# Optimization experiments

Measured on AMD Instinct MI355X. Metric: run time of the kernel, lower is better.

The kernel has to match this reference:

```python
import jax, jax.numpy as jnp
import numpy as np

B, N, C, K = 8, 4096, 128, 16
POOL_RATE = 4  # npoint = N // POOL_RATE


def setup_inputs() -> dict:
    key = jax.random.key(0)
    k1, k2, k3 = jax.random.split(key, 3)
    vertices = jax.random.normal(k1, (B, 3, N), dtype=jnp.float32)
    feature_map = jax.random.normal(k2, (B, C, N), dtype=jnp.float32)
    # pre-flattened global knn indices, values in [0, B*N) as produced upstream
    idx = jax.random.randint(k3, (B * N * K,), 0, B * N, dtype=jnp.int64)
    return {"vertices": vertices, "feature_map": feature_map, "idx": idx}


def farthest_point_sample(xyz, npoint):
    """xyz: (B, N, 3) -> centroid indices (B, npoint).
    Deterministic start at index 0 (torch version uses a random start)."""
    b, n, _ = xyz.shape

    def step(carry, _):
        distance, farthest = carry
        centroid = jnp.take_along_axis(xyz, farthest[:, None, None], axis=1)  # (B,1,3)
        dist = jnp.sum((xyz - centroid) ** 2, axis=-1)  # (B,N)
        distance = jnp.minimum(distance, dist)
        new_farthest = jnp.argmax(distance, axis=-1)
        return (distance, new_farthest), farthest

    dist0 = jnp.full((b, n), 1e10, dtype=xyz.dtype)
    far0 = jnp.zeros((b,), dtype=jnp.int32)
    _, cents = jax.lax.scan(step, (dist0, far0), None, length=npoint)
    return cents.T  # (B, npoint)


def reference(vertices, feature_map, idx):
    b, c, n = feature_map.shape
    # get_graph_feature with precomputed flat idx: gather neighbors then max-pool
    flat = feature_map.transpose(0, 2, 1).reshape(b * n, c)        # (B*N, C)
    neigh = flat[idx].reshape(b, n, K, c)                          # (B,N,K,C)
    pooled = jnp.max(neigh, axis=2)                                # (B,N,C) == (B,C,N) pooled_feature, channel-last

    npoint = n // POOL_RATE
    xyz = vertices.transpose(0, 2, 1)                              # (B,N,3)
    cents = farthest_point_sample(xyz, npoint)                     # (B,npoint)

    vertices_pool = jnp.take_along_axis(xyz, cents[:, :, None], axis=1).transpose(0, 2, 1)     # (B,3,npoint)
    feature_map_pool = jnp.take_along_axis(pooled, cents[:, :, None], axis=1).transpose(0, 2, 1)  # (B,C,npoint)
    return (vertices_pool, feature_map_pool)
```

## Files before the change

### kernel.cpp

```cpp
#include <hip/hip_runtime.h>
#include <hip/hip_bf16.h>
#include <math.h>

#define B_SZ 8
#define N_SZ 4096
#define C_SZ 128
#define K_SZ 16
#define NPOINT 1024

#define FPS_T 256
#define FPS_PAIRS 8

typedef float vf2 __attribute__((ext_vector_type(2)));

template <int CTRL>
__device__ __forceinline__ float dpp_fmax(float x) {
    int t = __builtin_amdgcn_update_dpp(0, __float_as_int(x), CTRL, 0xF, 0xF, true);
    return fmaxf(x, __int_as_float(t));
}
template <int CTRL>
__device__ __forceinline__ unsigned dpp_umin(unsigned x) {
    unsigned t = (unsigned)__builtin_amdgcn_update_dpp((int)0xFFFFFFFF, (int)x,
                                                       CTRL, 0xF, 0xF, false);
    return t < x ? t : x;
}
__device__ __forceinline__ float wave_fmax(float x) {
    x = dpp_fmax<0x111>(x);
    x = dpp_fmax<0x112>(x);
    x = dpp_fmax<0x114>(x);
    x = dpp_fmax<0x118>(x);
    x = dpp_fmax<0x142>(x);
    x = dpp_fmax<0x143>(x);
    return __int_as_float(__builtin_amdgcn_readlane(__float_as_int(x), 63));
}
__device__ __forceinline__ unsigned wave_umin(unsigned x) {
    x = dpp_umin<0x111>(x);
    x = dpp_umin<0x112>(x);
    x = dpp_umin<0x114>(x);
    x = dpp_umin<0x118>(x);
    x = dpp_umin<0x142>(x);
    x = dpp_umin<0x143>(x);
    return (unsigned)__builtin_amdgcn_readlane((int)x, 63);
}

__global__ void transpose_fm(const float* __restrict__ fm, float* __restrict__ fmT) {
    __shared__ float tile[32][33];
    const int b  = blockIdx.z;
    const int c0 = blockIdx.y * 32;
    const int n0 = blockIdx.x * 32;
    const int tx = threadIdx.x;
    const int ty = threadIdx.y;
    const float* p = fm + (size_t)b * C_SZ * N_SZ;
#pragma unroll
    for (int i = 0; i < 4; i++) {
        tile[ty + i * 8][tx] = p[(size_t)(c0 + ty + i * 8) * N_SZ + n0 + tx];
    }
    __syncthreads();
    float* q = fmT + (size_t)b * N_SZ * C_SZ;
#pragma unroll
    for (int i = 0; i < 4; i++) {
        q[(size_t)(n0 + ty + i * 8) * C_SZ + c0 + tx] = tile[tx][ty + i * 8];
    }
}

__global__ __launch_bounds__(FPS_T) void fps_kernel(
        const float* __restrict__ verts,
        float* __restrict__ out_vp,
        int* __restrict__ cents)
{
#pragma clang fp contract(off)
#pragma clang fp reassociate(off)
    __shared__ vf2   sxy[N_SZ];
    __shared__ float szz[N_SZ];
    __shared__ int   scent[NPOINT];
    __shared__ alignas(16) float cval[2][4];
    __shared__ alignas(16) int   cidx[2][4];

    const int b    = blockIdx.x;
    const int tid  = threadIdx.x;
    const int lane = tid & 63;
    const int wid  = tid >> 6;
    const float* vb = verts + (size_t)b * 3 * N_SZ;

    vf2 px[FPS_PAIRS], py[FPS_PAIRS], pz[FPS_PAIRS], dd[FPS_PAIRS];
#pragma unroll
    for (int p = 0; p < FPS_PAIRS; p++) {
        const int n0 = tid + (2 * p) * FPS_T;
        const int n1 = n0 + FPS_T;
        const float x0 = vb[n0],            x1 = vb[n1];
        const float y0 = vb[N_SZ + n0],     y1 = vb[N_SZ + n1];
        const float z0 = vb[2 * N_SZ + n0], z1 = vb[2 * N_SZ + n1];
        px[p] = (vf2){x0, x1};
        py[p] = (vf2){y0, y1};
        pz[p] = (vf2){z0, z1};
        dd[p] = (vf2){1e10f, 1e10f};
        sxy[n0] = (vf2){x0, y0}; szz[n0] = z0;
        sxy[n1] = (vf2){x1, y1}; szz[n1] = z1;
    }
    __syncthreads();

    int ci = 0;
    vf2 cxy = sxy[0];
    float cz = szz[0];

    for (int i = 0; i < NPOINT; i++) {
        if (tid == 0) scent[i] = ci;

        const vf2 cx2 = (vf2){cxy.x, cxy.x};
        const vf2 cy2 = (vf2){cxy.y, cxy.y};
        const vf2 cz2 = (vf2){cz, cz};

        float bv = -1.0f;
        int   bj = 0;
#pragma unroll
        for (int p = 0; p < FPS_PAIRS; p++) {
            const vf2 dx = px[p] - cx2;
            const vf2 dy = py[p] - cy2;
            const vf2 dz = pz[p] - cz2;
            vf2 s = dx * dx + dy * dy;
            s = s + dz * dz;
            vf2 d;
            d.x = fminf(dd[p].x, s.x);
            d.y = fminf(dd[p].y, s.y);
            dd[p] = d;
            if (d.x > bv) { bv = d.x; bj = 2 * p; }
            if (d.y > bv) { bv = d.y; bj = 2 * p + 1; }
        }
        const unsigned bn = (unsigned)(tid + (bj << 8));

        const float    wmax = wave_fmax(bv);
        const unsigned cand = (bv == wmax) ? bn : 0xFFFFFFFFu;
        const unsigned widx = wave_umin(cand);

        const int par = i & 1;
        if (lane == 0) { cval[par][wid] = wmax; cidx[par][wid] = (int)widx; }
        __syncthreads();

        const float4 vv = *(const float4*)&cval[par][0];
        const int4   jj = *(const int4*)&cidx[par][0];
        float v = vv.x; int ii = jj.x;
        if (vv.y > v || (vv.y == v && jj.y < ii)) { v = vv.y; ii = jj.y; }
        if (vv.z > v || (vv.z == v && jj.z < ii)) { v = vv.z; ii = jj.z; }
        if (vv.w > v || (vv.w == v && jj.w < ii)) { v = vv.w; ii = jj.w; }

        ci  = ii;
        cxy = sxy[ii];
        cz  = szz[ii];
    }
    __syncthreads();

    for (int i = tid; i < NPOINT; i += FPS_T) {
        const int c = scent[i];
        const vf2 xy = sxy[c];
        const float z = szz[c];
        cents[b * NPOINT + i] = c;
        out_vp[(b * 3 + 0) * NPOINT + i] = xy.x;
        out_vp[(b * 3 + 1) * NPOINT + i] = xy.y;
        out_vp[(b * 3 + 2) * NPOINT + i] = z;
    }
}

__global__ __launch_bounds__(256) void pool_gather(
        const float* __restrict__ fmT,
        const int* __restrict__ idx,
        const int* __restrict__ cents,
        float* __restrict__ pooled)
{
    const int wave = (int)((blockIdx.x * blockDim.x + threadIdx.x) >> 6);
    const int lane = threadIdx.x & 63;
    const int b = wave >> 10;
    const int ci = cents[wave];
    const int* ip = idx + ((size_t)(b * N_SZ + ci)) * K_SZ;
    const float2* src = (const float2*)fmT;

    float2 acc = make_float2(-INFINITY, -INFINITY);
#pragma unroll
    for (int k = 0; k < K_SZ; k++) {
        const int p = ip[k];
        const float2 v = src[(size_t)p * (C_SZ / 2) + lane];
        acc.x = fmaxf(acc.x, v.x);
        acc.y = fmaxf(acc.y, v.y);
    }
    ((float2*)pooled)[(size_t)wave * (C_SZ / 2) + lane] = acc;
}

__global__ void transpose_pooled(const float* __restrict__ pooled, float* __restrict__ out_fp) {
    __shared__ float tile[32][33];
    const int b  = blockIdx.z;
    const int c0 = blockIdx.y * 32;
    const int j0 = blockIdx.x * 32;
    const int tx = threadIdx.x;
    const int ty = threadIdx.y;
    const float* p = pooled + (size_t)b * NPOINT * C_SZ;
#pragma unroll
    for (int i = 0; i < 4; i++) {
        tile[ty + i * 8][tx] = p[(size_t)(j0 + ty + i * 8) * C_SZ + c0 + tx];
    }
    __syncthreads();
    float* q = out_fp + (size_t)b * C_SZ * NPOINT;
#pragma unroll
    for (int i = 0; i < 4; i++) {
        q[(size_t)(c0 + ty + i * 8) * NPOINT + j0 + tx] = tile[tx][ty + i * 8];
    }
}

extern "C" void kernel_launch(void* const* d_in, const int* in_sizes, int n_in,
                              void* d_out, int out_size, void* d_ws, size_t ws_size,
                              hipStream_t stream) {
    const float* verts = (const float*)d_in[0];
    const float* fm    = (const float*)d_in[1];
    const int*   idx   = (const int*)d_in[2];

    float* out    = (float*)d_out;
    float* out_vp = out;
    float* out_fp = out + (size_t)B_SZ * 3 * NPOINT;

    char* ws = (char*)d_ws;
    float* fmT    = (float*)ws;
    float* pooled = (float*)(ws + (size_t)B_SZ * N_SZ * C_SZ * 4);
    int*   cents  = (int*)(ws + (size_t)B_SZ * N_SZ * C_SZ * 4
                              + (size_t)B_SZ * NPOINT * C_SZ * 4);

    dim3 tb(32, 8);
    transpose_fm<<<dim3(N_SZ / 32, C_SZ / 32, B_SZ), tb, 0, stream>>>(fm, fmT);
    fps_kernel<<<B_SZ, FPS_T, 0, stream>>>(verts, out_vp, cents);
    pool_gather<<<(B_SZ * NPOINT) / 4, 256, 0, stream>>>(fmT, idx, cents, pooled);
    transpose_pooled<<<dim3(NPOINT / 32, C_SZ / 32, B_SZ), tb, 0, stream>>>(pooled, out_fp);
}
```

Baseline: 736.9 us.

## Pack FPS argmax into 64-bit key reduction, widen block, fuse gather-transpose

The FPS kernel now packs the distance bits and the inverted index into one 64-bit key. One DPP max-reduction therefore replaces the separate value-max and index-min passes per wave. The block also grows to 512 threads with 4 pairs each, cutting per-thread serial work per iteration at the cost of merging 8 wave results. Point coordinates move into a single float4 LDS array, and pool_gather now writes the transposed output through a shared tile, which removes the pooled intermediate buffer and one kernel launch.

```diff
diff --git a/kernel.cpp b/kernel.cpp
--- a/kernel.cpp
+++ b/kernel.cpp
@@ -8,39 +8,32 @@
 #define K_SZ 16
 #define NPOINT 1024
 
-#define FPS_T 256
-#define FPS_PAIRS 8
+#define FPS_T 512
+#define FPS_PAIRS 4
 
 typedef float vf2 __attribute__((ext_vector_type(2)));
 
 template <int CTRL>
-__device__ __forceinline__ float dpp_fmax(float x) {
-    int t = __builtin_amdgcn_update_dpp(0, __float_as_int(x), CTRL, 0xF, 0xF, true);
-    return fmaxf(x, __int_as_float(t));
-}
-template <int CTRL>
-__device__ __forceinline__ unsigned dpp_umin(unsigned x) {
-    unsigned t = (unsigned)__builtin_amdgcn_update_dpp((int)0xFFFFFFFF, (int)x,
-                                                       CTRL, 0xF, 0xF, false);
-    return t < x ? t : x;
-}
-__device__ __forceinline__ float wave_fmax(float x) {
-    x = dpp_fmax<0x111>(x);
-    x = dpp_fmax<0x112>(x);
-    x = dpp_fmax<0x114>(x);
-    x = dpp_fmax<0x118>(x);
-    x = dpp_fmax<0x142>(x);
-    x = dpp_fmax<0x143>(x);
-    return __int_as_float(__builtin_amdgcn_readlane(__float_as_int(x), 63));
-}
-__device__ __forceinline__ unsigned wave_umin(unsigned x) {
-    x = dpp_umin<0x111>(x);
-    x = dpp_umin<0x112>(x);
-    x = dpp_umin<0x114>(x);
-    x = dpp_umin<0x118>(x);
-    x = dpp_umin<0x142>(x);
-    x = dpp_umin<0x143>(x);
-    return (unsigned)__builtin_amdgcn_readlane((int)x, 63);
+__device__ __forceinline__ unsigned long long dpp_kmax_step(unsigned long long k) {
+    const unsigned lo = (unsigned)k;
+    const unsigned hi = (unsigned)(k >> 32);
+    const unsigned lo2 = (unsigned)__builtin_amdgcn_update_dpp(0, (int)lo, CTRL, 0xF, 0xF, true);
+    const unsigned hi2 = (unsigned)__builtin_amdgcn_update_dpp(0, (int)hi, CTRL, 0xF, 0xF, true);
+    const unsigned long long k2 = ((unsigned long long)hi2 << 32) | (unsigned long long)lo2;
+    return (k2 > k) ? k2 : k;
+}
+__device__ __forceinline__ unsigned long long wave_kmax63(unsigned long long k) {
+    k = dpp_kmax_step<0x111>(k);
+    k = dpp_kmax_step<0x112>(k);
+    k = dpp_kmax_step<0x114>(k);
+    k = dpp_kmax_step<0x118>(k);
+    k = dpp_kmax_step<0x142>(k);
+    k = dpp_kmax_step<0x143>(k);
+    return k;
+}
+__device__ __forceinline__ unsigned long long kmax2(unsigned long long a,
+                                                   unsigned long long b) {
+    return a > b ? a : b;
 }
 
 __global__ void transpose_fm(const float* __restrict__ fm, float* __restrict__ fmT) {
@@ -70,11 +63,9 @@
 {
 #pragma clang fp contract(off)
 #pragma clang fp reassociate(off)
-    __shared__ vf2   sxy[N_SZ];
-    __shared__ float szz[N_SZ];
-    __shared__ int   scent[NPOINT];
-    __shared__ alignas(16) float cval[2][4];
-    __shared__ alignas(16) int   cidx[2][4];
+    __shared__ float4 sp[N_SZ];
+    __shared__ int    scent[NPOINT];
+    __shared__ alignas(16) unsigned long long ckey[2][8];
 
     const int b    = blockIdx.x;
     const int tid  = threadIdx.x;
@@ -94,20 +85,20 @@
         py[p] = (vf2){y0, y1};
         pz[p] = (vf2){z0, z1};
         dd[p] = (vf2){1e10f, 1e10f};
-        sxy[n0] = (vf2){x0, y0}; szz[n0] = z0;
-        sxy[n1] = (vf2){x1, y1}; szz[n1] = z1;
+        sp[n0] = make_float4(x0, y0, z0, 0.0f);
+        sp[n1] = make_float4(x1, y1, z1, 0.0f);
     }
     __syncthreads();
 
     int ci = 0;
-    vf2 cxy = sxy[0];
-    float cz = szz[0];
+    float4 c0 = sp[0];
+    float cx = c0.x, cy = c0.y, cz = c0.z;
 
     for (int i = 0; i < NPOINT; i++) {
         if (tid == 0) scent[i] = ci;
 
-        const vf2 cx2 = (vf2){cxy.x, cxy.x};
-        const vf2 cy2 = (vf2){cxy.y, cxy.y};
+        const vf2 cx2 = (vf2){cx, cx};
+        const vf2 cy2 = (vf2){cy, cy};
         const vf2 cz2 = (vf2){cz, cz};
 
         float bv = -1.0f;
@@ -126,51 +117,56 @@
             if (d.x > bv) { bv = d.x; bj = 2 * p; }
             if (d.y > bv) { bv = d.y; bj = 2 * p + 1; }
         }
-        const unsigned bn = (unsigned)(tid + (bj << 8));
-
-        const float    wmax = wave_fmax(bv);
-        const unsigned cand = (bv == wmax) ? bn : 0xFFFFFFFFu;
-        const unsigned widx = wave_umin(cand);
-
+        const unsigned n = (unsigned)(tid + (bj << 9));
+        unsigned long long key =
+            ((unsigned long long)__float_as_uint(bv) << 32) |
+            (unsigned long long)(4095u - n);
+
+        key = wave_kmax63(key);
         const int par = i & 1;
-        if (lane == 0) { cval[par][wid] = wmax; cidx[par][wid] = (int)widx; }
+        if (lane == 63) ckey[par][wid] = key;
         __syncthreads();
 
-        const float4 vv = *(const float4*)&cval[par][0];
-        const int4   jj = *(const int4*)&cidx[par][0];
-        float v = vv.x; int ii = jj.x;
-        if (vv.y > v || (vv.y == v && jj.y < ii)) { v = vv.y; ii = jj.y; }
-        if (vv.z > v || (vv.z == v && jj.z < ii)) { v = vv.z; ii = jj.z; }
-        if (vv.w > v || (vv.w == v && jj.w < ii)) { v = vv.w; ii = jj.w; }
-
-        ci  = ii;
-        cxy = sxy[ii];
-        cz  = szz[ii];
+        const ulonglong2* kb = (const ulonglong2*)(&ckey[par][0]);
+        const ulonglong2 a0 = kb[0], a1 = kb[1], a2 = kb[2], a3 = kb[3];
+        const unsigned long long m0 = kmax2(a0.x, a0.y);
+        const unsigned long long m1 = kmax2(a1.x, a1.y);
+        const unsigned long long m2 = kmax2(a2.x, a2.y);
+        const unsigned long long m3 = kmax2(a3.x, a3.y);
+        const unsigned long long kk = kmax2(kmax2(m0, m1), kmax2(m2, m3));
+
+        ci = (int)(4095u - (unsigned)kk);
+        const float4 c = sp[ci];
+        cx = c.x; cy = c.y; cz = c.z;
     }
     __syncthreads();
 
     for (int i = tid; i < NPOINT; i += FPS_T) {
-        const int c = scent[i];
-        const vf2 xy = sxy[c];
-        const float z = szz[c];
-        cents[b * NPOINT + i] = c;
-        out_vp[(b * 3 + 0) * NPOINT + i] = xy.x;
-        out_vp[(b * 3 + 1) * NPOINT + i] = xy.y;
-        out_vp[(b * 3 + 2) * NPOINT + i] = z;
-    }
-}
-
-__global__ __launch_bounds__(256) void pool_gather(
+        const int cc = scent[i];
+        const float4 v = sp[cc];
+        cents[b * NPOINT + i] = cc;
+        out_vp[(b * 3 + 0) * NPOINT + i] = v.x;
+        out_vp[(b * 3 + 1) * NPOINT + i] = v.y;
+        out_vp[(b * 3 + 2) * NPOINT + i] = v.z;
+    }
+}
+
+#define GT_J 16
+__global__ __launch_bounds__(1024) void pool_gather_t(
         const float* __restrict__ fmT,
         const int* __restrict__ idx,
         const int* __restrict__ cents,
-        float* __restrict__ pooled)
+        float* __restrict__ out_fp)
 {
-    const int wave = (int)((blockIdx.x * blockDim.x + threadIdx.x) >> 6);
-    const int lane = threadIdx.x & 63;
-    const int b = wave >> 10;
-    const int ci = cents[wave];
-    const int* ip = idx + ((size_t)(b * N_SZ + ci)) * K_SZ;
+    __shared__ float tile[C_SZ][GT_J + 1];
+    const int tid  = threadIdx.x;
+    const int lane = tid & 63;
+    const int w    = tid >> 6;
+    const int j0   = blockIdx.x * GT_J;
+    const int gp   = j0 + w;
+    const int b    = gp >> 10;
+    const int ci   = cents[gp];
+    const int* ip  = idx + ((size_t)(b * N_SZ + ci)) * K_SZ;
     const float2* src = (const float2*)fmT;
 
     float2 acc = make_float2(-INFINITY, -INFINITY);
@@ -181,26 +177,17 @@
         acc.x = fmaxf(acc.x, v.x);
         acc.y = fmaxf(acc.y, v.y);
     }
-    ((float2*)pooled)[(size_t)wave * (C_SZ / 2) + lane] = acc;
-}
-
-__global__ void transpose_pooled(const float* __restrict__ pooled, float* __restrict__ out_fp) {
-    __shared__ float tile[32][33];
-    const int b  = blockIdx.z;
-    const int c0 = blockIdx.y * 32;
-    const int j0 = blockIdx.x * 32;
-    const int tx = threadIdx.x;
-    const int ty = threadIdx.y;
-    const float* p = pooled + (size_t)b * NPOINT * C_SZ;
-#pragma unroll
-    for (int i = 0; i < 4; i++) {
-        tile[ty + i * 8][tx] = p[(size_t)(j0 + ty + i * 8) * C_SZ + c0 + tx];
-    }
-    __syncthreads();
-    float* q = out_fp + (size_t)b * C_SZ * NPOINT;
-#pragma unroll
-    for (int i = 0; i < 4; i++) {
-        q[(size_t)(c0 + ty + i * 8) * NPOINT + j0 + tx] = tile[tx][ty + i * 8];
+    tile[2 * lane][w]     = acc.x;
+    tile[2 * lane + 1][w] = acc.y;
+    __syncthreads();
+
+    float* q = out_fp + (size_t)b * C_SZ * NPOINT + (j0 & (NPOINT - 1));
+#pragma unroll
+    for (int it = 0; it < 2; it++) {
+        const int e  = tid + it * 1024;
+        const int c  = e >> 4;
+        const int jj = e & (GT_J - 1);
+        q[(size_t)c * NPOINT + jj] = tile[c][jj];
     }
 }
 
@@ -216,14 +203,11 @@
     float* out_fp = out + (size_t)B_SZ * 3 * NPOINT;
 
     char* ws = (char*)d_ws;
-    float* fmT    = (float*)ws;
-    float* pooled = (float*)(ws + (size_t)B_SZ * N_SZ * C_SZ * 4);
-    int*   cents  = (int*)(ws + (size_t)B_SZ * N_SZ * C_SZ * 4
-                              + (size_t)B_SZ * NPOINT * C_SZ * 4);
+    float* fmT   = (float*)ws;
+    int*   cents = (int*)(ws + (size_t)B_SZ * N_SZ * C_SZ * 4);
 
     dim3 tb(32, 8);
     transpose_fm<<<dim3(N_SZ / 32, C_SZ / 32, B_SZ), tb, 0, stream>>>(fm, fmT);
     fps_kernel<<<B_SZ, FPS_T, 0, stream>>>(verts, out_vp, cents);
-    pool_gather<<<(B_SZ * NPOINT) / 4, 256, 0, stream>>>(fmT, idx, cents, pooled);
-    transpose_pooled<<<dim3(NPOINT / 32, C_SZ / 32, B_SZ), tb, 0, stream>>>(pooled, out_fp);
-}
+    pool_gather_t<<<(B_SZ * NPOINT) / GT_J, 1024, 0, stream>>>(fmT, idx, cents, out_fp);
+}
```

Result: faster. 698.1 us (-5.3%).
